# Performance work log

Hardware: AMD Instinct MI355X
Metric: run time of the kernel (lower is better)

## Reference

```python
import jax, jax.numpy as jnp
import numpy as np

N_NODES = 100000


def gcn_conv(x, W, src, dst, n):
    """PyG GCNConv with bias=False: add self-loops, symmetric norm, scatter-add."""
    h = x @ W  # [N, out]
    # degree including self-loop (all edge weights = 1)
    deg = jnp.zeros((n,), dtype=x.dtype).at[dst].add(1.0) + 1.0
    inv_sqrt = jax.lax.rsqrt(deg)  # deg >= 1 so safe
    edge_norm = inv_sqrt[src] * inv_sqrt[dst]  # [E]
    # neighbor aggregation: out_i = sum_{j->i} norm_ji * h_j
    agg = jnp.zeros_like(h).at[dst].add(h[src] * edge_norm[:, None])
    # self-loop contribution: norm_ii = 1/deg_i
    return agg + h * (inv_sqrt * inv_sqrt)[:, None]


def setup_inputs() -> dict:
    key = jax.random.key(0)
    k1, k2, k3, k4 = jax.random.split(key, 4)
    x = jax.random.normal(k1, (N_NODES, 128), dtype=jnp.float32)
    edge_index = jax.random.randint(k2, (2, 1600000), 0, N_NODES, dtype=jnp.int32)
    W1 = jax.random.normal(k3, (128, 64), dtype=jnp.float32) * (1.0 / np.sqrt(128))
    W2 = jax.random.normal(k4, (64, 40), dtype=jnp.float32) * (1.0 / np.sqrt(64))
    return {"x": x, "edge_index": edge_index, "W1": W1, "W2": W2}


def reference(x, edge_index, W1, W2):
    n = x.shape[0]
    src, dst = edge_index[0], edge_index[1]
    # layer 1 (dropout p=0.0 is identity) + relu
    h = jax.nn.relu(gcn_conv(x, W1, src, dst, n))
    # layer 2 + relu, then squeeze
    out = jax.nn.relu(gcn_conv(h, W2, src, dst, n))
    return jnp.squeeze(out)
```

## Files before the change

### kernel.cpp

```cpp
#include <hip/hip_runtime.h>
#include <hip/hip_fp16.h>


#define F0 128
#define F1 64
#define F2 40
#define SCAN_B 512
#define GEMM_BLKS 768
#define NRANK (GEMM_BLKS / 3)
#define STG_GM 512

__global__ void k_zero(int* __restrict__ cnt, int n) {
    const int i = blockIdx.x * blockDim.x + threadIdx.x;
    if (i < n) cnt[i] = 0;
}

__global__ __launch_bounds__(256) void k_gemmrank(const float* __restrict__ x,
                                                  const float* __restrict__ W,
                                                  __half* __restrict__ h,
                                                  const int* __restrict__ ei,
                                                  int* __restrict__ cnt,
                                                  int* __restrict__ rank,
                                                  int n, int E) {
    __shared__ float Wl[F0 * F1];
    __shared__ float xs[32 * F0];
    const int bid = blockIdx.x;
    const int tid = threadIdx.x;

    if ((bid % 3) == 2) {
        const int rb = bid / 3;
        const int stride = NRANK * 256;
#pragma unroll 4
        for (int e = rb * 256 + tid; e < E; e += stride)
            rank[e] = atomicAdd(&cnt[ei[E + e]], 1);
        return;
    }

    const int gid = bid - bid / 3;
    const int c = tid & 63;
    const int rq = tid >> 6;

    {
        float4* Wl4 = (float4*)Wl;
        const float4* Wg4 = (const float4*)W;
#pragma unroll
        for (int j = 0; j < (F0 * F1 / 4) / 256; ++j)
            Wl4[j * 256 + tid] = Wg4[j * 256 + tid];
    }
    __syncthreads();

    const int NG = GEMM_BLKS - NRANK;
    const int ntiles = (n + 31) >> 5;
    for (int tile = gid; tile < ntiles; tile += NG) {
        float4* xs4w = (float4*)xs;
#pragma unroll
        for (int j = 0; j < 4; ++j) {
            int fi = j * 256 + tid;
            int row = fi >> 5;
            int rg = tile * 32 + row;
            if (rg > n - 1) rg = n - 1;
            const float4* xrow = (const float4*)(x + (long long)rg * F0);
            xs4w[fi] = xrow[fi & 31];
        }
        __syncthreads();

        float acc[8] = {0.f,0.f,0.f,0.f,0.f,0.f,0.f,0.f};
#pragma unroll 2
        for (int b = 0; b < 32; ++b) {
            const float w0 = Wl[(4 * b + 0) * F1 + c];
            const float w1 = Wl[(4 * b + 1) * F1 + c];
            const float w2 = Wl[(4 * b + 2) * F1 + c];
            const float w3 = Wl[(4 * b + 3) * F1 + c];
#pragma unroll
            for (int i = 0; i < 8; ++i) {
                float4 xv = ((const float4*)xs)[(rq * 8 + i) * 32 + b];
                acc[i] = fmaf(xv.w, w3, fmaf(xv.z, w2, fmaf(xv.y, w1, fmaf(xv.x, w0, acc[i]))));
            }
        }

#pragma unroll
        for (int i = 0; i < 8; ++i) {
            int rg = tile * 32 + rq * 8 + i;
            if (rg < n) h[(long long)rg * F1 + c] = __float2half(acc[i]);
        }
        __syncthreads();
    }
}

__global__ __launch_bounds__(SCAN_B) void k_rsqrt_bsum(const int* __restrict__ cnt,
                                                       float* __restrict__ invs,
                                                       int* __restrict__ bsum, int n) {
    __shared__ int s[SCAN_B];
    const int t = threadIdx.x;
    const int i = blockIdx.x * SCAN_B + t;
    int c = 0;
    if (i < n) {
        c = cnt[i];
        invs[i] = rsqrtf((float)(c + 1));
    }
    s[t] = c;
    __syncthreads();
    for (int off = SCAN_B / 2; off > 0; off >>= 1) {
        if (t < off) s[t] += s[t + off];
        __syncthreads();
    }
    if (t == 0) bsum[blockIdx.x] = s[0];
}

__global__ __launch_bounds__(1024) void k_bscan(int* __restrict__ bsum, int nb) {
    __shared__ int s[1024];
    const int t = threadIdx.x;
    const int orig = (t < nb) ? bsum[t] : 0;
    s[t] = orig;
    __syncthreads();
    for (int off = 1; off < 1024; off <<= 1) {
        int add = (t >= off) ? s[t - off] : 0;
        __syncthreads();
        s[t] += add;
        __syncthreads();
    }
    if (t < nb) bsum[t] = s[t] - orig;
}

__global__ __launch_bounds__(SCAN_B) void k_scan3(const int* __restrict__ cnt,
                                                  const int* __restrict__ bsum,
                                                  int* __restrict__ rowptr, int n) {
    __shared__ int s[SCAN_B];
    const int t = threadIdx.x;
    const int i = blockIdx.x * SCAN_B + t;
    const int orig = (i < n) ? cnt[i] : 0;
    s[t] = orig;
    __syncthreads();
    for (int off = 1; off < SCAN_B; off <<= 1) {
        int add = (t >= off) ? s[t - off] : 0;
        __syncthreads();
        s[t] += add;
        __syncthreads();
    }
    const int excl = s[t] - orig + bsum[blockIdx.x];
    if (i < n) rowptr[i] = excl;
    if (i == n - 1) rowptr[n] = excl + orig;
}


__device__ __forceinline__ void fill_body(const int* __restrict__ ei,
                                          const int* __restrict__ rank,
                                          const int* __restrict__ rowptr,
                                          int* __restrict__ csr4,
                                          int E, int flo, int fhi, int relbid,
                                          int tid) {
    int e = relbid * 1024 + tid;
#pragma unroll
    for (int j = 0; j < 4; ++j, e += 256) {
        if (e < E) {
            const int d = ei[E + e];
            if (d >= flo && d < fhi)
                csr4[rowptr[d] + rank[e]] = ei[e];
        }
    }
}

__device__ __forceinline__ void gemm2_body(const float* __restrict__ g,
                                           const float* __restrict__ W,
                                           const float* __restrict__ invs,
                                           __half* __restrict__ h,
                                           int n, int lo, int hi,
                                           int relbid, int nblk, int tid) {
    __shared__ float Wl[F1 * F2];
    __shared__ float xs[32 * F1];
    const int c = tid & 63;
    const int rq = tid >> 6;

    for (int i = tid; i < F1 * F2; i += 256) Wl[i] = W[i];
    __syncthreads();

    const int t0 = lo >> 5;
    const int ntiles = (hi - lo + 31) >> 5;
    for (int ti = relbid; ti < ntiles; ti += nblk) {
        const int tile = t0 + ti;
        float4* xs4w = (float4*)xs;
#pragma unroll
        for (int j = 0; j < 2; ++j) {
            int fi = j * 256 + tid;
            int row = fi >> 4;
            int rg = tile * 32 + row;
            if (rg > n - 1) rg = n - 1;
            const float4* xrow = (const float4*)(g + (long long)rg * F1);
            xs4w[fi] = xrow[fi & 15];
        }
        __syncthreads();

        if (c < F2) {
            float acc[8] = {0.f,0.f,0.f,0.f,0.f,0.f,0.f,0.f};
#pragma unroll 2
            for (int b = 0; b < 16; ++b) {
                const float w0 = Wl[(4 * b + 0) * F2 + c];
                const float w1 = Wl[(4 * b + 1) * F2 + c];
                const float w2 = Wl[(4 * b + 2) * F2 + c];
                const float w3 = Wl[(4 * b + 3) * F2 + c];
#pragma unroll
                for (int i = 0; i < 8; ++i) {
                    float4 xv = ((const float4*)xs)[(rq * 8 + i) * 16 + b];
                    acc[i] = fmaf(xv.w, w3, fmaf(xv.z, w2, fmaf(xv.y, w1, fmaf(xv.x, w0, acc[i]))));
                }
            }
#pragma unroll
            for (int i = 0; i < 8; ++i) {
                int rg = tile * 32 + rq * 8 + i;
                if (rg < hi) h[(long long)rg * F2 + c] = __float2half(acc[i] * invs[rg]);
            }
        }
        __syncthreads();
    }
}

__device__ __forceinline__ void gather64_body(const int* __restrict__ rowptr,
                                              const int* __restrict__ csr4,
                                              const float* __restrict__ invs,
                                              const __half* __restrict__ h,
                                              float* __restrict__ g,
                                              int lo, int hi, int relbid, int tid) {
    const int w = lo + relbid * 4 + (tid >> 6);
    const int lane = tid & 63;
    if (w >= hi) return;
    const int beg = rowptr[w];
    const int end = rowptr[w + 1];
    float acc0 = 0.f, acc1 = 0.f, acc2 = 0.f, acc3 = 0.f;
    int k = beg;
    for (; k + 8 <= end; k += 8) {
        const int s0 = csr4[k+0], s1 = csr4[k+1], s2 = csr4[k+2], s3 = csr4[k+3];
        const int s4 = csr4[k+4], s5 = csr4[k+5], s6 = csr4[k+6], s7 = csr4[k+7];
        const float v0 = __half2float(h[(long long)s0 * F1 + lane]);
        const float v1 = __half2float(h[(long long)s1 * F1 + lane]);
        const float v2 = __half2float(h[(long long)s2 * F1 + lane]);
        const float v3 = __half2float(h[(long long)s3 * F1 + lane]);
        const float v4 = __half2float(h[(long long)s4 * F1 + lane]);
        const float v5 = __half2float(h[(long long)s5 * F1 + lane]);
        const float v6 = __half2float(h[(long long)s6 * F1 + lane]);
        const float v7 = __half2float(h[(long long)s7 * F1 + lane]);
        acc0 += v0 + v4; acc1 += v1 + v5; acc2 += v2 + v6; acc3 += v3 + v7;
    }
    for (; k + 2 <= end; k += 2) {
        const int s0 = csr4[k], s1 = csr4[k+1];
        acc0 += __half2float(h[(long long)s0 * F1 + lane]);
        acc1 += __half2float(h[(long long)s1 * F1 + lane]);
    }
    if (k < end) {
        acc0 += __half2float(h[(long long)csr4[k] * F1 + lane]);
    }
    const float iv = invs[w];
    const float self = __half2float(h[(long long)w * F1 + lane]);
    g[(long long)w * F1 + lane] = fmaxf(iv * (((acc0 + acc1) + (acc2 + acc3)) + self), 0.f);
}


__global__ void k_fill_scale(const int* __restrict__ ei, const int* __restrict__ rank,
                             const int* __restrict__ rowptr, int* __restrict__ csr4,
                             __half* __restrict__ h, const float* __restrict__ invs,
                             int E, int n, int flo, int fhi, int gFILL) {
    const int bid = blockIdx.x;
    const int tid = threadIdx.x;
    if (bid < gFILL) {
        fill_body(ei, rank, rowptr, csr4, E, flo, fhi, bid, tid);
    } else {
        const int fb = bid - gFILL;
        const long long total4 = (long long)n * F1 / 4;
        long long i4 = (long long)fb * 256 + tid;
        const long long stride = (long long)2048 * 256;
        for (; i4 < total4; i4 += stride) {
            const int r = (int)(i4 >> 4);
            const float iv = invs[r];
            __half2* hp = (__half2*)h + i4 * 2;
            __half2 a = hp[0], b = hp[1];
            float2 af = __half22float2(a), bf = __half22float2(b);
            af.x *= iv; af.y *= iv; bf.x *= iv; bf.y *= iv;
            hp[0] = __float22half2_rn(af);
            hp[1] = __float22half2_rn(bf);
        }
    }
}

__global__ __launch_bounds__(256, 8) void k_stage(const float* __restrict__ g1,
                                                  const float* __restrict__ W2,
                                                  const float* __restrict__ invs,
                                                  __half* __restrict__ h2,
                                                  const int* __restrict__ ei,
                                                  const int* __restrict__ rank,
                                                  const int* __restrict__ rowptr,
                                                  int* __restrict__ csr4,
                                                  const __half* __restrict__ h1,
                                                  float* __restrict__ g1out,
                                                  int n, int E,
                                                  int nGm, int gmlo, int gmhi,
                                                  int nFill, int flo, int fhi,
                                                  int g64lo, int g64hi) {
    const int bid = blockIdx.x;
    const int tid = threadIdx.x;
    if (bid < nGm) {
        gemm2_body(g1, W2, invs, h2, n, gmlo, gmhi, bid, nGm, tid);
    } else if (bid < nGm + nFill) {
        fill_body(ei, rank, rowptr, csr4, E, flo, fhi, bid - nGm, tid);
    } else {
        gather64_body(rowptr, csr4, invs, h1, g1out, g64lo, g64hi,
                      bid - nGm - nFill, tid);
    }
}

__global__ __launch_bounds__(256) void k_gemm2(const float* __restrict__ g,
                                               const float* __restrict__ W,
                                               const float* __restrict__ invs,
                                               __half* __restrict__ h,
                                               int n, int lo, int hi) {
    gemm2_body(g, W, invs, h, n, lo, hi, blockIdx.x, gridDim.x, threadIdx.x);
}

__global__ __launch_bounds__(256) void k_gather40(const int* __restrict__ rowptr,
                                                  const int* __restrict__ csr4,
                                                  const float* __restrict__ invs,
                                                  const __half* __restrict__ h,
                                                  float* __restrict__ g, int n) {
    const int w = (blockIdx.x * blockDim.x + threadIdx.x) >> 6;
    const int lane = threadIdx.x & 63;
    if (w >= n) return;
    const int beg = rowptr[w];
    const int end = rowptr[w + 1];
    float acc0 = 0.f, acc1 = 0.f, acc2 = 0.f, acc3 = 0.f;
    int k = beg;
    if (lane < F2) {
        for (; k + 8 <= end; k += 8) {
            const int s0 = csr4[k+0], s1 = csr4[k+1], s2 = csr4[k+2], s3 = csr4[k+3];
            const int s4 = csr4[k+4], s5 = csr4[k+5], s6 = csr4[k+6], s7 = csr4[k+7];
            const float v0 = __half2float(h[(long long)s0 * F2 + lane]);
            const float v1 = __half2float(h[(long long)s1 * F2 + lane]);
            const float v2 = __half2float(h[(long long)s2 * F2 + lane]);
            const float v3 = __half2float(h[(long long)s3 * F2 + lane]);
            const float v4 = __half2float(h[(long long)s4 * F2 + lane]);
            const float v5 = __half2float(h[(long long)s5 * F2 + lane]);
            const float v6 = __half2float(h[(long long)s6 * F2 + lane]);
            const float v7 = __half2float(h[(long long)s7 * F2 + lane]);
            acc0 += v0 + v4; acc1 += v1 + v5; acc2 += v2 + v6; acc3 += v3 + v7;
        }
        for (; k + 2 <= end; k += 2) {
            const int s0 = csr4[k], s1 = csr4[k+1];
            acc0 += __half2float(h[(long long)s0 * F2 + lane]);
            acc1 += __half2float(h[(long long)s1 * F2 + lane]);
        }
        if (k < end) {
            acc0 += __half2float(h[(long long)csr4[k] * F2 + lane]);
        }
        const float iv = invs[w];
        const float self = __half2float(h[(long long)w * F2 + lane]);
        g[(long long)w * F2 + lane] = fmaxf(iv * (((acc0 + acc1) + (acc2 + acc3)) + self), 0.f);
    }
}

extern "C" void kernel_launch(void* const* d_in, const int* in_sizes, int n_in,
                              void* d_out, int out_size, void* d_ws, size_t ws_size,
                              hipStream_t stream) {
    const float* x  = (const float*)d_in[0];
    const int*   ei = (const int*)d_in[1];
    const float* W1 = (const float*)d_in[2];
    const float* W2 = (const float*)d_in[3];
    float* out = (float*)d_out;
    const int n = in_sizes[0] / F0;
    const int E = in_sizes[1] / 2;

    const size_t np = ((size_t)n + 65) & ~(size_t)63;
    char* wsb = (char*)d_ws;
    int*    cnt    = (int*)wsb;
    int*    rowptr = cnt + np;
    float*  invs   = (float*)(rowptr + np);
    int*    rank   = (int*)(invs + np);
    int*    csr4   = rank + E;
    __half* h1h    = (__half*)(csr4 + E);
    float*  g1     = (float*)(h1h + (size_t)n * F1);
    __half* h2h    = (__half*)(g1 + (size_t)n * F1);
    int*    bsum   = (int*)(h2h + (size_t)n * F2);

    const int nh = ((n / 2 + 31) / 32) * 32;
    const int nb = (n + SCAN_B - 1) / SCAN_B;
    const int gN = (n + 255) / 256;
    const int gFILL = (E + 1023) / 1024;
    const int nA = (nh + 3) / 4;
    const int nB = (n - nh + 3) / 4;
    const int gW = (int)(((long long)n * 64 + 255) / 256);

    hipLaunchKernelGGL(k_zero,      dim3(gN), dim3(256), 0, stream, cnt, n);
    hipLaunchKernelGGL(k_gemmrank,  dim3(GEMM_BLKS), dim3(256), 0, stream,
                       x, W1, h1h, ei, cnt, rank, n, E);
    hipLaunchKernelGGL(k_rsqrt_bsum, dim3(nb), dim3(SCAN_B), 0, stream, cnt, invs, bsum, n);
    hipLaunchKernelGGL(k_bscan,      dim3(1),  dim3(1024), 0, stream, bsum, nb);
    hipLaunchKernelGGL(k_scan3,      dim3(nb), dim3(SCAN_B), 0, stream, cnt, bsum, rowptr, n);

    hipLaunchKernelGGL(k_fill_scale, dim3(gFILL + 2048), dim3(256), 0, stream,
                       ei, rank, rowptr, csr4, h1h, invs, E, n, 0, nh, gFILL);
    hipLaunchKernelGGL(k_stage, dim3(gFILL + nA), dim3(256), 0, stream,
                       g1, W2, invs, h2h, ei, rank, rowptr, csr4, h1h, g1,
                       n, E, 0, 0, 0, gFILL, nh, n, 0, nh);
    hipLaunchKernelGGL(k_stage, dim3(STG_GM + nB), dim3(256), 0, stream,
                       g1, W2, invs, h2h, ei, rank, rowptr, csr4, h1h, g1,
                       n, E, STG_GM, 0, nh, 0, 0, 0, nh, n);
    hipLaunchKernelGGL(k_gemm2, dim3(GEMM_BLKS), dim3(256), 0, stream,
                       g1, W2, invs, h2h, n, nh, n);
    hipLaunchKernelGGL(k_gather40, dim3(gW), dim3(256), 0, stream,
                       rowptr, csr4, invs, h2h, out, n);
}
```

Baseline: 252.4 us.

## Do full CSR fill in one pass instead of splitting across stages

```diff
diff --git a/kernel.cpp b/kernel.cpp
--- a/kernel.cpp
+++ b/kernel.cpp
@@ -142,23 +142,6 @@
     if (i == n - 1) rowptr[n] = excl + orig;
 }
 
-
-__device__ __forceinline__ void fill_body(const int* __restrict__ ei,
-                                          const int* __restrict__ rank,
-                                          const int* __restrict__ rowptr,
-                                          int* __restrict__ csr4,
-                                          int E, int flo, int fhi, int relbid,
-                                          int tid) {
-    int e = relbid * 1024 + tid;
-#pragma unroll
-    for (int j = 0; j < 4; ++j, e += 256) {
-        if (e < E) {
-            const int d = ei[E + e];
-            if (d >= flo && d < fhi)
-                csr4[rowptr[d] + rank[e]] = ei[e];
-        }
-    }
-}
 
 __device__ __forceinline__ void gemm2_body(const float* __restrict__ g,
                                            const float* __restrict__ W,
@@ -257,11 +240,19 @@
 __global__ void k_fill_scale(const int* __restrict__ ei, const int* __restrict__ rank,
                              const int* __restrict__ rowptr, int* __restrict__ csr4,
                              __half* __restrict__ h, const float* __restrict__ invs,
-                             int E, int n, int flo, int fhi, int gFILL) {
+                             int E, int n, int gFILL) {
     const int bid = blockIdx.x;
     const int tid = threadIdx.x;
     if (bid < gFILL) {
-        fill_body(ei, rank, rowptr, csr4, E, flo, fhi, bid, tid);
+        int e = bid * 1024 + tid;
+#pragma unroll
+        for (int j = 0; j < 4; ++j, e += 256) {
+            if (e < E) {
+                const int s = ei[e];
+                const int d = ei[E + e];
+                csr4[rowptr[d] + rank[e]] = s;
+            }
+        }
     } else {
         const int fb = bid - gFILL;
         const long long total4 = (long long)n * F1 / 4;
@@ -280,29 +271,32 @@
     }
 }
 
+__global__ __launch_bounds__(256) void k_gather64(const int* __restrict__ rowptr,
+                                                  const int* __restrict__ csr4,
+                                                  const float* __restrict__ invs,
+                                                  const __half* __restrict__ h,
+                                                  float* __restrict__ g,
+                                                  int lo, int hi) {
+    gather64_body(rowptr, csr4, invs, h, g, lo, hi, blockIdx.x, threadIdx.x);
+}
+
 __global__ __launch_bounds__(256, 8) void k_stage(const float* __restrict__ g1,
                                                   const float* __restrict__ W2,
                                                   const float* __restrict__ invs,
                                                   __half* __restrict__ h2,
-                                                  const int* __restrict__ ei,
-                                                  const int* __restrict__ rank,
                                                   const int* __restrict__ rowptr,
-                                                  int* __restrict__ csr4,
+                                                  const int* __restrict__ csr4,
                                                   const __half* __restrict__ h1,
                                                   float* __restrict__ g1out,
-                                                  int n, int E,
+                                                  int n,
                                                   int nGm, int gmlo, int gmhi,
-                                                  int nFill, int flo, int fhi,
                                                   int g64lo, int g64hi) {
     const int bid = blockIdx.x;
     const int tid = threadIdx.x;
     if (bid < nGm) {
         gemm2_body(g1, W2, invs, h2, n, gmlo, gmhi, bid, nGm, tid);
-    } else if (bid < nGm + nFill) {
-        fill_body(ei, rank, rowptr, csr4, E, flo, fhi, bid - nGm, tid);
     } else {
-        gather64_body(rowptr, csr4, invs, h1, g1out, g64lo, g64hi,
-                      bid - nGm - nFill, tid);
+        gather64_body(rowptr, csr4, invs, h1, g1out, g64lo, g64hi, bid - nGm, tid);
     }
 }
 
@@ -393,13 +387,12 @@
     hipLaunchKernelGGL(k_scan3,      dim3(nb), dim3(SCAN_B), 0, stream, cnt, bsum, rowptr, n);
 
     hipLaunchKernelGGL(k_fill_scale, dim3(gFILL + 2048), dim3(256), 0, stream,
-                       ei, rank, rowptr, csr4, h1h, invs, E, n, 0, nh, gFILL);
-    hipLaunchKernelGGL(k_stage, dim3(gFILL + nA), dim3(256), 0, stream,
-                       g1, W2, invs, h2h, ei, rank, rowptr, csr4, h1h, g1,
-                       n, E, 0, 0, 0, gFILL, nh, n, 0, nh);
+                       ei, rank, rowptr, csr4, h1h, invs, E, n, gFILL);
+    hipLaunchKernelGGL(k_gather64, dim3(nA), dim3(256), 0, stream,
+                       rowptr, csr4, invs, h1h, g1, 0, nh);
     hipLaunchKernelGGL(k_stage, dim3(STG_GM + nB), dim3(256), 0, stream,
-                       g1, W2, invs, h2h, ei, rank, rowptr, csr4, h1h, g1,
-                       n, E, STG_GM, 0, nh, 0, 0, 0, nh, n);
+                       g1, W2, invs, h2h, rowptr, csr4, h1h, g1,
+                       n, STG_GM, 0, nh, nh, n);
     hipLaunchKernelGGL(k_gemm2, dim3(GEMM_BLKS), dim3(256), 0, stream,
                        g1, W2, invs, h2h, n, nh, n);
     hipLaunchKernelGGL(k_gather40, dim3(gW), dim3(256), 0, stream,
```

Result: no change. 250.1 us (-0.9%).
